# Kernel tuning notes

Measured on AMD Instinct MI355X. Metric: run time of the kernel, lower is better.

The kernel has to match this reference:

```python
import jax, jax.numpy as jnp
import numpy as np
from jax import lax

N = 100000   # n_nodes
E = 600000   # n_edges (no self loops by construction)
D = 128      # hidden_dim
L = 3        # n_hops
K = 5        # tail_k_threshold


def setup_inputs() -> dict:
    key = jax.random.key(0)
    ks = jax.random.split(key, 10)
    x = jax.random.normal(ks[0], (N, D), dtype=jnp.float32)
    src = jax.random.randint(ks[1], (E,), 0, N)
    off = jax.random.randint(ks[2], (E,), 1, N)
    dst = (src + off) % N  # guarantees dst != src (self loops removed in original)
    s = 1.0 / np.sqrt(D)
    def U(k, shape):
        return jax.random.uniform(k, shape, minval=-s, maxval=s, dtype=jnp.float32)
    return {
        "x": x,
        "G1": U(ks[3], (L, D, D)), "G2": U(ks[4], (L, D, D)),
        "B1": U(ks[5], (L, D, D)), "B2": U(ks[6], (L, D, D)),
        "R": U(ks[7], (L, D)),
        "edge_src": src, "edge_dst": dst,
    }


def _lrelu(v):
    return jax.nn.leaky_relu(v, 0.2)


def reference(x, G1, G2, B1, B2, R, edge_src, edge_dst):
    # row degrees of adj (A[src, dst] = 1)
    deg = jax.ops.segment_sum(jnp.ones(E, jnp.float32), edge_src, num_segments=N)
    inv_d = jnp.where(deg > 0, 1.0 / jnp.maximum(deg, 1.0), 0.0)   # left norm D^-1 A
    inv_d1 = 1.0 / (deg + 1.0)                                      # (A+I) left norm
    inv_d2 = 1.0 / (deg + 2.0)                                      # +1 virtual node
    w0, w1, w2 = inv_d[edge_src], inv_d1[edge_src], inv_d2[edge_src]
    head_mask = deg > K

    def spmm(w_edge, h):  # (D^-1 A) @ h via gather-scale-scatter
        return jax.ops.segment_sum(w_edge[:, None] * h[edge_dst], edge_src, num_segments=N)

    def propagate(head):
        h = x
        embs = [h]
        sups = []
        for l in range(L):
            nb = spmm(w0, h)
            ft = lax.stop_gradient(h)
            nbd = lax.stop_gradient(nb)
            gamma = _lrelu(ft @ G1[l].T + nbd @ G2[l].T) + 1.0
            beta = _lrelu(ft @ B1[l].T + nbd @ B2[l].T)
            m = ft + gamma * R[l] + beta - nbd   # missing_info (Relation, ablation=0)
            sups.append(m)
            if head:
                h = spmm(w1, h) + inv_d1[:, None] * h
            else:
                h = spmm(w2, h) + inv_d2[:, None] * h + m * inv_d2[:, None]
            embs.append(h)
        emb = jnp.mean(jnp.stack(embs, 0), 0)
        sup = jnp.mean(jnp.stack(sups, 0), 0)
        return emb, sup

    emb_h, _ = propagate(True)
    emb_t, _ = propagate(False)
    node_emb = jnp.where(head_mask[:, None], emb_h, emb_t)
    return node_emb
```

## Files before the change

kernel.cpp:

```cpp
#include <hip/hip_runtime.h>

#define N_NODES 100000
#define N_EDGES 600000
#define DIM 128
#define SCAN_B 1024
#define NCHUNK 98

typedef __attribute__((ext_vector_type(4))) float f32x4;
typedef __attribute__((ext_vector_type(8))) short bf16x8;
typedef __attribute__((ext_vector_type(4))) unsigned short u16x4;
typedef __attribute__((ext_vector_type(8))) unsigned short u16x8;

__device__ __forceinline__ unsigned short f2bf(float f) {
    union { float f; unsigned u; } cv; cv.f = f;
    unsigned r = (cv.u + 0x7FFFu + ((cv.u >> 16) & 1u)) >> 16;
    return (unsigned short)r;
}
__device__ __forceinline__ float bf2f(unsigned short v) {
    union { unsigned u; float f; } c; c.u = ((unsigned)v) << 16; return c.f;
}


__global__ void k_degree(const int* __restrict__ src, int* __restrict__ degi) {
    int e = blockIdx.x * 256 + threadIdx.x;
    if (e < N_EDGES) atomicAdd(&degi[src[e]], 1);
}

__global__ void k_chunksum(const int* __restrict__ degi, int* __restrict__ bsum) {
    __shared__ int sm[SCAN_B];
    int i = blockIdx.x * SCAN_B + threadIdx.x;
    sm[threadIdx.x] = (i < N_NODES) ? degi[i] : 0;
    __syncthreads();
    for (int s = SCAN_B / 2; s > 0; s >>= 1) {
        if (threadIdx.x < (unsigned)s) sm[threadIdx.x] += sm[threadIdx.x + s];
        __syncthreads();
    }
    if (threadIdx.x == 0) bsum[blockIdx.x] = sm[0];
}

__global__ void k_scanb(int* __restrict__ bsum, int nb) {
    __shared__ int sm[128];
    int t = threadIdx.x;
    int v = (t < nb) ? bsum[t] : 0;
    sm[t] = v; __syncthreads();
    for (int s = 1; s < 128; s <<= 1) {
        int a = (t >= s) ? sm[t - s] : 0;
        __syncthreads();
        sm[t] += a;
        __syncthreads();
    }
    if (t < nb) bsum[t] = sm[t] - v;
}

__global__ void k_rowptr(const int* __restrict__ degi, const int* __restrict__ bsum,
                         int* __restrict__ rowptr, int* __restrict__ cnt,
                         float* __restrict__ inv0, float* __restrict__ inv1,
                         float* __restrict__ inv2) {
    __shared__ int sm[SCAN_B];
    int i = blockIdx.x * SCAN_B + threadIdx.x;
    int v = (i < N_NODES) ? degi[i] : 0;
    sm[threadIdx.x] = v; __syncthreads();
    for (int s = 1; s < SCAN_B; s <<= 1) {
        int a = (threadIdx.x >= (unsigned)s) ? sm[threadIdx.x - s] : 0;
        __syncthreads();
        sm[threadIdx.x] += a;
        __syncthreads();
    }
    if (i < N_NODES) {
        int excl = bsum[blockIdx.x] + sm[threadIdx.x] - v;
        rowptr[i] = excl;
        cnt[i] = excl;
        float d = (float)v;
        inv0[i] = (v > 0) ? 1.0f / d : 0.0f;
        inv1[i] = 1.0f / (d + 1.0f);
        inv2[i] = 1.0f / (d + 2.0f);
    }
}

__global__ void k_fill(const int* __restrict__ src, const int* __restrict__ dst,
                       int* __restrict__ cnt, int* __restrict__ col) {
    int e = blockIdx.x * 256 + threadIdx.x;
    if (e < N_EDGES) {
        int pos = atomicAdd(&cnt[src[e]], 1);
        col[pos] = dst[e];
    }
}

__global__ void k_pack(const float* __restrict__ G1, const float* __restrict__ G2,
                       const float* __restrict__ B1, const float* __restrict__ B2,
                       short* __restrict__ Wp) {
    int idx = blockIdx.x * 256 + threadIdx.x;
    int j = idx & 7, lane = (idx >> 3) & 63, nt = (idx >> 9) & 15, kb = (idx >> 13) & 7, l = idx >> 16;
    int k = kb * 32 + (lane >> 4) * 8 + j;
    int n = nt * 16 + (lane & 15);
    float v;
    if (n < 128) {
        v = (k < 128) ? G1[(l * 128 + n) * 128 + k] : G2[(l * 128 + n) * 128 + (k - 128)];
    } else {
        int n2 = n - 128;
        v = (k < 128) ? B1[(l * 128 + n2) * 128 + k] : B2[(l * 128 + n2) * 128 + (k - 128)];
    }
    Wp[idx] = (short)f2bf(v);
}

__global__ void k_xcast(const float* __restrict__ x, unsigned short* __restrict__ xb) {
    int i = (blockIdx.x * 256 + threadIdx.x) * 4;
    f32x4 v = *(const f32x4*)(x + i);
    unsigned short o0 = f2bf(v[0]), o1 = f2bf(v[1]), o2 = f2bf(v[2]), o3 = f2bf(v[3]);
    unsigned long long pk = (unsigned long long)o0 | ((unsigned long long)o1 << 16)
                          | ((unsigned long long)o2 << 32) | ((unsigned long long)o3 << 48);
    *(unsigned long long*)(xb + i) = pk;
}


template <int NE>
__device__ __forceinline__ void gath_issue(const u16x8* __restrict__ h8,
        int idx, int base, int c, int d, float* acc) {
    u16x8 v[NE];
#pragma unroll
    for (int e = 0; e < NE; ++e) {
        int ce = __shfl(idx, base + e, 64);
        v[e] = h8[(size_t)ce * 16 + c];
    }
#pragma unroll
    for (int e = 0; e < NE; ++e) {
        if (e < d) {
#pragma unroll
            for (int j = 0; j < 8; ++j) acc[j] += bf2f(v[e][j]);
        }
    }
}

__device__ __forceinline__ void gather4(const u16x8* __restrict__ h8,
        const int* __restrict__ col, int start, int d, int lane, float* acc) {
    int c = lane & 15;
    int base = lane & 48;
    int dd = d < 16 ? d : 16;
    int idx = (c < dd) ? col[start + c] : 0;
    int dm = d;
    int tmx = __shfl_xor(dm, 16);
    dm = dm > tmx ? dm : tmx;
    tmx = __shfl_xor(dm, 32);
    dm = dm > tmx ? dm : tmx;
    if (dm <= 8) {
        gath_issue<8>(h8, idx, base, c, d, acc);
    } else {
        gath_issue<16>(h8, idx, base, c, d, acc);
        if (dm > 16) {
            for (int e = 16; e < d; ++e) {
                int c0 = col[start + e];
                u16x8 v = h8[(size_t)c0 * 16 + c];
#pragma unroll
                for (int j = 0; j < 8; ++j) acc[j] += bf2f(v[j]);
            }
        }
    }
}


__device__ __forceinline__ void tail_block(
    int rb,
    unsigned short (*sH)[136], unsigned short (*sS)[136], unsigned short (*sO)[136],
    const unsigned short* __restrict__ hb,
    unsigned short* __restrict__ hA, int write_hA,
    unsigned short* __restrict__ hb_next,
    const unsigned short* __restrict__ xb, const unsigned short* __restrict__ t1b,
    float* __restrict__ outp,
    const float* __restrict__ Rl, const short* __restrict__ Wp,
    const float* __restrict__ inv0, const float* __restrict__ inv1,
    const float* __restrict__ inv2,
    const int* __restrict__ rowptr, const int* __restrict__ degi,
    const int* __restrict__ col, int last)
{
    int wave = threadIdx.x >> 6, lane = threadIdx.x & 63;

    {
        int g = lane >> 4, c = lane & 15;
        int row = rb + wave * 4 + g;
        int start = rowptr[row], d = degi[row];
        u16x8 hv = ((const u16x8*)hb)[(size_t)row * 16 + c];
        float acc[8] = {0,0,0,0,0,0,0,0};
        gather4((const u16x8*)hb, col, start, d, lane, acc);
        u16x8 so;
#pragma unroll
        for (int j = 0; j < 8; ++j) so[j] = f2bf(acc[j]);
        *(u16x8*)&sS[wave * 4 + g][c * 8] = so;
        *(u16x8*)&sH[wave * 4 + g][c * 8] = hv;
        if (write_hA) {
            float w1 = inv1[row];
            u16x8 ho;
#pragma unroll
            for (int j = 0; j < 8; ++j) ho[j] = f2bf(w1 * (acc[j] + bf2f(hv[j])));
            ((u16x8*)hA)[(size_t)row * 16 + c] = ho;
        }
    }
    __syncthreads();

    int q = lane >> 4, m = lane & 15;
    float w0 = inv0[rb + m];
    const short* wl = Wp + lane * 8;

    const f32x4 vz = {0.f, 0.f, 0.f, 0.f};
    f32x4 aA[2] = {vz, vz}, aB[2] = {vz, vz};

#pragma unroll
    for (int kb = 0; kb < 4; ++kb) {
        bf16x8 ah = *(const bf16x8*)&sH[m][kb * 32 + q * 8];
#pragma unroll
        for (int j = 0; j < 2; ++j) {
            bf16x8 b1v = *(const bf16x8*)(wl + (kb * 16 + 2 * wave + j) * 512);
            bf16x8 b2v = *(const bf16x8*)(wl + (kb * 16 + 2 * wave + 8 + j) * 512);
            aA[j] = __builtin_amdgcn_mfma_f32_16x16x32_bf16(ah, b1v, aA[j], 0, 0, 0);
            aB[j] = __builtin_amdgcn_mfma_f32_16x16x32_bf16(ah, b2v, aB[j], 0, 0, 0);
        }
    }
#pragma unroll
    for (int kb = 0; kb < 4; ++kb) {
        u16x8 sv = *(const u16x8*)&sS[m][kb * 32 + q * 8];
        bf16x8 as;
#pragma unroll
        for (int j = 0; j < 8; ++j) as[j] = (short)f2bf(w0 * bf2f(sv[j]));
#pragma unroll
        for (int j = 0; j < 2; ++j) {
            bf16x8 b1v = *(const bf16x8*)(wl + ((kb + 4) * 16 + 2 * wave + j) * 512);
            bf16x8 b2v = *(const bf16x8*)(wl + ((kb + 4) * 16 + 2 * wave + 8 + j) * 512);
            aA[j] = __builtin_amdgcn_mfma_f32_16x16x32_bf16(as, b1v, aA[j], 0, 0, 0);
            aB[j] = __builtin_amdgcn_mfma_f32_16x16x32_bf16(as, b2v, aB[j], 0, 0, 0);
        }
    }

    float Rv[2];
#pragma unroll
    for (int j = 0; j < 2; ++j) Rv[j] = Rl[(2 * wave + j) * 16 + m];

#pragma unroll
    for (int r = 0; r < 4; ++r) {
        int gi = rb + q * 4 + r;
        float wi0 = inv0[gi], wi2 = inv2[gi];
        int dgi = degi[gi];
#pragma unroll
        for (int j = 0; j < 2; ++j) {
            int cc = (2 * wave + j) * 16 + m;
            float z1 = aA[j][r], z2 = aB[j][r];
            float h = bf2f(sH[q * 4 + r][cc]);
            float sva = bf2f(sS[q * 4 + r][cc]);
            float ga = (z1 > 0.f ? z1 : 0.2f * z1) + 1.0f;
            float be = (z2 > 0.f ? z2 : 0.2f * z2);
            float mm = h + ga * Rv[j] + be - wi0 * sva;
            float hn = wi2 * (sva + h + mm);
            if (!last) {
                sO[q * 4 + r][cc] = f2bf(hn);
            } else if (dgi <= 5) {
                float xv = bf2f(xb[(size_t)gi * DIM + cc]);
                float t1 = bf2f(t1b[(size_t)gi * DIM + cc]);
                outp[(size_t)gi * DIM + cc] = 0.25f * (xv + t1 + h + hn);
            }
        }
    }
    if (!last) {
        __syncthreads();
        int g = lane >> 4, c = lane & 15;
        int row = rb + wave * 4 + g;
        ((u16x8*)hb_next)[(size_t)row * 16 + c] = *(u16x8*)&sO[wave * 4 + g][c * 8];
    }
}

__device__ __forceinline__ void head_block(
    int rb,
    const unsigned short* __restrict__ hsrc, unsigned short* __restrict__ hnext,
    const unsigned short* __restrict__ xb, const unsigned short* __restrict__ h1b,
    float* __restrict__ outp, const float* __restrict__ inv1,
    const int* __restrict__ rowptr, const int* __restrict__ degi,
    const int* __restrict__ col, int final_hop)
{
    int wave = threadIdx.x >> 6, lane = threadIdx.x & 63;
    int g = lane >> 4, c = lane & 15;
    int row = rb + wave * 4 + g;
    int start = rowptr[row], d = degi[row];
    u16x8 hv = ((const u16x8*)hsrc)[(size_t)row * 16 + c];
    float acc[8] = {0,0,0,0,0,0,0,0};
    gather4((const u16x8*)hsrc, col, start, d, lane, acc);
    float w = inv1[row];
    float hn[8];
#pragma unroll
    for (int j = 0; j < 8; ++j) hn[j] = w * (acc[j] + bf2f(hv[j]));
    if (!final_hop) {
        u16x8 ho;
#pragma unroll
        for (int j = 0; j < 8; ++j) ho[j] = f2bf(hn[j]);
        ((u16x8*)hnext)[(size_t)row * 16 + c] = ho;
    } else if (d > 5) {
        u16x8 xv = ((const u16x8*)xb)[(size_t)row * 16 + c];
        u16x8 h1 = ((const u16x8*)h1b)[(size_t)row * 16 + c];
        f32x4 e0, e1;
#pragma unroll
        for (int j = 0; j < 4; ++j)
            e0[j] = 0.25f * (bf2f(xv[j]) + bf2f(h1[j]) + bf2f(hv[j]) + hn[j]);
#pragma unroll
        for (int j = 0; j < 4; ++j)
            e1[j] = 0.25f * (bf2f(xv[4 + j]) + bf2f(h1[4 + j]) + bf2f(hv[4 + j]) + hn[4 + j]);
        float* op = outp + (size_t)row * DIM + c * 8;
        *(f32x4*)op = e0;
        *(f32x4*)(op + 4) = e1;
    }
}


__global__ __launch_bounds__(256, 4) void k_fused0(
    const unsigned short* __restrict__ xb, unsigned short* __restrict__ hA,
    unsigned short* __restrict__ tA, float* __restrict__ outp,
    const float* __restrict__ Rl, const short* __restrict__ Wp,
    const float* __restrict__ inv0, const float* __restrict__ inv1,
    const float* __restrict__ inv2,
    const int* __restrict__ rowptr, const int* __restrict__ degi,
    const int* __restrict__ col)
{
    __shared__ __align__(16) unsigned short sH[16][136], sS[16][136], sO[16][136];
    tail_block(blockIdx.x * 16, sH, sS, sO, xb, hA, 1, tA, xb, tA, outp,
               Rl, Wp, inv0, inv1, inv2, rowptr, degi, col, 0);
}

__global__ __launch_bounds__(256, 4) void k_tail(
    const unsigned short* __restrict__ tb, unsigned short* __restrict__ tb_next,
    const unsigned short* __restrict__ xb, const unsigned short* __restrict__ t1b,
    float* __restrict__ outp,
    const float* __restrict__ Rl, const short* __restrict__ Wp,
    const float* __restrict__ inv0, const float* __restrict__ inv1,
    const float* __restrict__ inv2,
    const int* __restrict__ rowptr, const int* __restrict__ degi,
    const int* __restrict__ col, int last)
{
    __shared__ __align__(16) unsigned short sH[16][136], sS[16][136], sO[16][136];
    tail_block(blockIdx.x * 16, sH, sS, sO, tb, (unsigned short*)0, 0, tb_next,
               xb, t1b, outp, Rl, Wp, inv0, inv1, inv2, rowptr, degi, col, last);
}

__global__ __launch_bounds__(256, 4) void k_head(
    const unsigned short* __restrict__ hsrc, unsigned short* __restrict__ hnext,
    const unsigned short* __restrict__ xb, const unsigned short* __restrict__ h1b,
    float* __restrict__ outp, const float* __restrict__ inv1,
    const int* __restrict__ rowptr, const int* __restrict__ degi,
    const int* __restrict__ col, int final_hop)
{
    head_block(blockIdx.x * 16, hsrc, hnext, xb, h1b, outp, inv1,
               rowptr, degi, col, final_hop);
}


extern "C" void kernel_launch(void* const* d_in, const int* in_sizes, int n_in,
                              void* d_out, int out_size, void* d_ws, size_t ws_size,
                              hipStream_t stream) {
    const float* x  = (const float*)d_in[0];
    const float* G1 = (const float*)d_in[1];
    const float* G2 = (const float*)d_in[2];
    const float* B1 = (const float*)d_in[3];
    const float* B2 = (const float*)d_in[4];
    const float* R  = (const float*)d_in[5];
    const int* esrc = (const int*)d_in[6];
    const int* edst = (const int*)d_in[7];
    float* out = (float*)d_out;

    char* base = (char*)d_ws;
    size_t off = 0;
    auto alloc = [&](size_t b) -> void* {
        void* p = base + off;
        off = (off + b + 255) & ~(size_t)255;
        return p;
    };
    int* degi   = (int*)alloc(4 * N_NODES);
    int* rowptr = (int*)alloc(4 * N_NODES);
    int* cnt    = (int*)alloc(4 * N_NODES);
    int* bsum   = (int*)alloc(4 * 256);
    int* col    = (int*)alloc(4 * N_EDGES);
    float* inv0 = (float*)alloc(4 * N_NODES);
    float* inv1 = (float*)alloc(4 * N_NODES);
    float* inv2 = (float*)alloc(4 * N_NODES);
    short* Wp   = (short*)alloc(2 * 3 * 65536);
    unsigned short* xb = (unsigned short*)alloc(2ull * N_NODES * DIM);
    unsigned short* hA = (unsigned short*)alloc(2ull * N_NODES * DIM);
    unsigned short* hB = (unsigned short*)alloc(2ull * N_NODES * DIM);
    unsigned short* tA = (unsigned short*)alloc(2ull * N_NODES * DIM);
    unsigned short* tB = (unsigned short*)alloc(2ull * N_NODES * DIM);

    hipMemsetAsync(degi, 0, 4 * N_NODES, stream);
    k_degree<<<(N_EDGES + 255) / 256, 256, 0, stream>>>(esrc, degi);
    k_chunksum<<<NCHUNK, SCAN_B, 0, stream>>>(degi, bsum);
    k_scanb<<<1, 128, 0, stream>>>(bsum, NCHUNK);
    k_rowptr<<<NCHUNK, SCAN_B, 0, stream>>>(degi, bsum, rowptr, cnt, inv0, inv1, inv2);
    k_fill<<<(N_EDGES + 255) / 256, 256, 0, stream>>>(esrc, edst, cnt, col);
    k_pack<<<768, 256, 0, stream>>>(G1, G2, B1, B2, Wp);
    k_xcast<<<12500, 256, 0, stream>>>(x, xb);

    k_fused0<<<6250, 256, 0, stream>>>(xb, hA, tA, out, R, Wp,
                                       inv0, inv1, inv2, rowptr, degi, col);

    k_head<<<6250, 256, 0, stream>>>(hA, hB, xb, hA, out, inv1, rowptr, degi, col, 0);
    k_head<<<6250, 256, 0, stream>>>(hB, hB, xb, hA, out, inv1, rowptr, degi, col, 1);

    k_tail<<<6250, 256, 0, stream>>>(tA, tB, xb, tA, out, R + 128, Wp + 65536,
                                     inv0, inv1, inv2, rowptr, degi, col, 0);
    k_tail<<<6250, 256, 0, stream>>>(tB, tB, xb, tA, out, R + 256, Wp + 131072,
                                     inv0, inv1, inv2, rowptr, degi, col, 1);
}
```

Before: 403.7 us.

## Fuse head and tail hop kernels into one dual-gather kernel per hop

Merges the separate head and tail propagation kernels for hops 2 and 3 into a single kernel that gathers neighbour rows from both the head and tail buffers using the same column indices. This shares the CSR index loads and rowptr/degree reads and cuts kernel launches from four to two. The cost is doubled register pressure in the gather (two accumulator sets and two loaded vectors per edge), which may lower occupancy. In-place reuse of tB/hB on the last hop is avoided by passing null next-buffers.

```diff
diff --git a/kernel.cpp b/kernel.cpp
--- a/kernel.cpp
+++ b/kernel.cpp
@@ -157,45 +157,73 @@
     }
 }
 
-
-__device__ __forceinline__ void tail_block(
+template <int NE>
+__device__ __forceinline__ void gath_issue2(const u16x8* __restrict__ hT,
+        const u16x8* __restrict__ hH,
+        int idx, int base, int c, int d, int e0, float* accT, float* accH) {
+    u16x8 vT[NE], vH[NE];
+#pragma unroll
+    for (int e = 0; e < NE; ++e) {
+        int ce = __shfl(idx, base + e0 + e, 64);
+        vT[e] = hT[(size_t)ce * 16 + c];
+        vH[e] = hH[(size_t)ce * 16 + c];
+    }
+#pragma unroll
+    for (int e = 0; e < NE; ++e) {
+        if (e0 + e < d) {
+#pragma unroll
+            for (int j = 0; j < 8; ++j) {
+                accT[j] += bf2f(vT[e][j]);
+                accH[j] += bf2f(vH[e][j]);
+            }
+        }
+    }
+}
+
+__device__ __forceinline__ void gather4_dual(const u16x8* __restrict__ hT,
+        const u16x8* __restrict__ hH,
+        const int* __restrict__ col, int start, int d, int lane,
+        float* accT, float* accH) {
+    int c = lane & 15;
+    int base = lane & 48;
+    int dd = d < 16 ? d : 16;
+    int idx = (c < dd) ? col[start + c] : 0;
+    int dm = d;
+    int tmx = __shfl_xor(dm, 16);
+    dm = dm > tmx ? dm : tmx;
+    tmx = __shfl_xor(dm, 32);
+    dm = dm > tmx ? dm : tmx;
+    if (dm <= 8) {
+        gath_issue2<8>(hT, hH, idx, base, c, d, 0, accT, accH);
+    } else {
+        gath_issue2<8>(hT, hH, idx, base, c, d, 0, accT, accH);
+        gath_issue2<8>(hT, hH, idx, base, c, d, 8, accT, accH);
+        if (dm > 16) {
+            for (int e = 16; e < d; ++e) {
+                int c0 = col[start + e];
+                u16x8 vT = hT[(size_t)c0 * 16 + c];
+                u16x8 vH = hH[(size_t)c0 * 16 + c];
+#pragma unroll
+                for (int j = 0; j < 8; ++j) {
+                    accT[j] += bf2f(vT[j]);
+                    accH[j] += bf2f(vH[j]);
+                }
+            }
+        }
+    }
+}
+
+__device__ __forceinline__ void tail_gemm(
     int rb,
     unsigned short (*sH)[136], unsigned short (*sS)[136], unsigned short (*sO)[136],
-    const unsigned short* __restrict__ hb,
-    unsigned short* __restrict__ hA, int write_hA,
     unsigned short* __restrict__ hb_next,
     const unsigned short* __restrict__ xb, const unsigned short* __restrict__ t1b,
     float* __restrict__ outp,
     const float* __restrict__ Rl, const short* __restrict__ Wp,
-    const float* __restrict__ inv0, const float* __restrict__ inv1,
-    const float* __restrict__ inv2,
-    const int* __restrict__ rowptr, const int* __restrict__ degi,
-    const int* __restrict__ col, int last)
+    const float* __restrict__ inv0, const float* __restrict__ inv2,
+    const int* __restrict__ degi, int last)
 {
     int wave = threadIdx.x >> 6, lane = threadIdx.x & 63;
-
-    {
-        int g = lane >> 4, c = lane & 15;
-        int row = rb + wave * 4 + g;
-        int start = rowptr[row], d = degi[row];
-        u16x8 hv = ((const u16x8*)hb)[(size_t)row * 16 + c];
-        float acc[8] = {0,0,0,0,0,0,0,0};
-        gather4((const u16x8*)hb, col, start, d, lane, acc);
-        u16x8 so;
-#pragma unroll
-        for (int j = 0; j < 8; ++j) so[j] = f2bf(acc[j]);
-        *(u16x8*)&sS[wave * 4 + g][c * 8] = so;
-        *(u16x8*)&sH[wave * 4 + g][c * 8] = hv;
-        if (write_hA) {
-            float w1 = inv1[row];
-            u16x8 ho;
-#pragma unroll
-            for (int j = 0; j < 8; ++j) ho[j] = f2bf(w1 * (acc[j] + bf2f(hv[j])));
-            ((u16x8*)hA)[(size_t)row * 16 + c] = ho;
-        }
-    }
-    __syncthreads();
-
     int q = lane >> 4, m = lane & 15;
     float w0 = inv0[rb + m];
     const short* wl = Wp + lane * 8;
@@ -265,46 +293,6 @@
     }
 }
 
-__device__ __forceinline__ void head_block(
-    int rb,
-    const unsigned short* __restrict__ hsrc, unsigned short* __restrict__ hnext,
-    const unsigned short* __restrict__ xb, const unsigned short* __restrict__ h1b,
-    float* __restrict__ outp, const float* __restrict__ inv1,
-    const int* __restrict__ rowptr, const int* __restrict__ degi,
-    const int* __restrict__ col, int final_hop)
-{
-    int wave = threadIdx.x >> 6, lane = threadIdx.x & 63;
-    int g = lane >> 4, c = lane & 15;
-    int row = rb + wave * 4 + g;
-    int start = rowptr[row], d = degi[row];
-    u16x8 hv = ((const u16x8*)hsrc)[(size_t)row * 16 + c];
-    float acc[8] = {0,0,0,0,0,0,0,0};
-    gather4((const u16x8*)hsrc, col, start, d, lane, acc);
-    float w = inv1[row];
-    float hn[8];
-#pragma unroll
-    for (int j = 0; j < 8; ++j) hn[j] = w * (acc[j] + bf2f(hv[j]));
-    if (!final_hop) {
-        u16x8 ho;
-#pragma unroll
-        for (int j = 0; j < 8; ++j) ho[j] = f2bf(hn[j]);
-        ((u16x8*)hnext)[(size_t)row * 16 + c] = ho;
-    } else if (d > 5) {
-        u16x8 xv = ((const u16x8*)xb)[(size_t)row * 16 + c];
-        u16x8 h1 = ((const u16x8*)h1b)[(size_t)row * 16 + c];
-        f32x4 e0, e1;
-#pragma unroll
-        for (int j = 0; j < 4; ++j)
-            e0[j] = 0.25f * (bf2f(xv[j]) + bf2f(h1[j]) + bf2f(hv[j]) + hn[j]);
-#pragma unroll
-        for (int j = 0; j < 4; ++j)
-            e1[j] = 0.25f * (bf2f(xv[4 + j]) + bf2f(h1[4 + j]) + bf2f(hv[4 + j]) + hn[4 + j]);
-        float* op = outp + (size_t)row * DIM + c * 8;
-        *(f32x4*)op = e0;
-        *(f32x4*)(op + 4) = e1;
-    }
-}
-
 
 __global__ __launch_bounds__(256, 4) void k_fused0(
     const unsigned short* __restrict__ xb, unsigned short* __restrict__ hA,
@@ -316,14 +304,35 @@
     const int* __restrict__ col)
 {
     __shared__ __align__(16) unsigned short sH[16][136], sS[16][136], sO[16][136];
-    tail_block(blockIdx.x * 16, sH, sS, sO, xb, hA, 1, tA, xb, tA, outp,
-               Rl, Wp, inv0, inv1, inv2, rowptr, degi, col, 0);
-}
-
-__global__ __launch_bounds__(256, 4) void k_tail(
+    int rb = blockIdx.x * 16;
+    int wave = threadIdx.x >> 6, lane = threadIdx.x & 63;
+    {
+        int g = lane >> 4, c = lane & 15;
+        int row = rb + wave * 4 + g;
+        int start = rowptr[row], d = degi[row];
+        u16x8 hv = ((const u16x8*)xb)[(size_t)row * 16 + c];
+        float acc[8] = {0,0,0,0,0,0,0,0};
+        gather4((const u16x8*)xb, col, start, d, lane, acc);
+        u16x8 so;
+#pragma unroll
+        for (int j = 0; j < 8; ++j) so[j] = f2bf(acc[j]);
+        *(u16x8*)&sS[wave * 4 + g][c * 8] = so;
+        *(u16x8*)&sH[wave * 4 + g][c * 8] = hv;
+        float w1 = inv1[row];
+        u16x8 ho;
+#pragma unroll
+        for (int j = 0; j < 8; ++j) ho[j] = f2bf(w1 * (acc[j] + bf2f(hv[j])));
+        ((u16x8*)hA)[(size_t)row * 16 + c] = ho;
+    }
+    __syncthreads();
+    tail_gemm(rb, sH, sS, sO, tA, xb, tA, outp, Rl, Wp, inv0, inv2, degi, 0);
+}
+
+__global__ __launch_bounds__(256, 4) void k_hop(
     const unsigned short* __restrict__ tb, unsigned short* __restrict__ tb_next,
+    const unsigned short* __restrict__ hb, unsigned short* __restrict__ hb_next,
     const unsigned short* __restrict__ xb, const unsigned short* __restrict__ t1b,
-    float* __restrict__ outp,
+    const unsigned short* __restrict__ h1b, float* __restrict__ outp,
     const float* __restrict__ Rl, const short* __restrict__ Wp,
     const float* __restrict__ inv0, const float* __restrict__ inv1,
     const float* __restrict__ inv2,
@@ -331,19 +340,53 @@
     const int* __restrict__ col, int last)
 {
     __shared__ __align__(16) unsigned short sH[16][136], sS[16][136], sO[16][136];
-    tail_block(blockIdx.x * 16, sH, sS, sO, tb, (unsigned short*)0, 0, tb_next,
-               xb, t1b, outp, Rl, Wp, inv0, inv1, inv2, rowptr, degi, col, last);
-}
-
-__global__ __launch_bounds__(256, 4) void k_head(
-    const unsigned short* __restrict__ hsrc, unsigned short* __restrict__ hnext,
-    const unsigned short* __restrict__ xb, const unsigned short* __restrict__ h1b,
-    float* __restrict__ outp, const float* __restrict__ inv1,
-    const int* __restrict__ rowptr, const int* __restrict__ degi,
-    const int* __restrict__ col, int final_hop)
-{
-    head_block(blockIdx.x * 16, hsrc, hnext, xb, h1b, outp, inv1,
-               rowptr, degi, col, final_hop);
+    int rb = blockIdx.x * 16;
+    int wave = threadIdx.x >> 6, lane = threadIdx.x & 63;
+
+    {
+        int g = lane >> 4, c = lane & 15;
+        int row = rb + wave * 4 + g;
+        int start = rowptr[row], d = degi[row];
+        u16x8 tv = ((const u16x8*)tb)[(size_t)row * 16 + c];
+        u16x8 hv = ((const u16x8*)hb)[(size_t)row * 16 + c];
+        float accT[8] = {0,0,0,0,0,0,0,0};
+        float accH[8] = {0,0,0,0,0,0,0,0};
+        gather4_dual((const u16x8*)tb, (const u16x8*)hb, col, start, d, lane, accT, accH);
+
+        u16x8 so;
+#pragma unroll
+        for (int j = 0; j < 8; ++j) so[j] = f2bf(accT[j]);
+        *(u16x8*)&sS[wave * 4 + g][c * 8] = so;
+        *(u16x8*)&sH[wave * 4 + g][c * 8] = tv;
+
+        float w1 = inv1[row];
+        if (!last) {
+            u16x8 ho;
+#pragma unroll
+            for (int j = 0; j < 8; ++j) ho[j] = f2bf(w1 * (accH[j] + bf2f(hv[j])));
+            ((u16x8*)hb_next)[(size_t)row * 16 + c] = ho;
+        } else if (d > 5) {
+            u16x8 xv = ((const u16x8*)xb)[(size_t)row * 16 + c];
+            u16x8 h1 = ((const u16x8*)h1b)[(size_t)row * 16 + c];
+            f32x4 e0, e1;
+#pragma unroll
+            for (int j = 0; j < 4; ++j) {
+                float h2 = bf2f(hv[j]);
+                e0[j] = 0.25f * (bf2f(xv[j]) + bf2f(h1[j]) + h2 + w1 * (accH[j] + h2));
+            }
+#pragma unroll
+            for (int j = 0; j < 4; ++j) {
+                float h2 = bf2f(hv[4 + j]);
+                e1[j] = 0.25f * (bf2f(xv[4 + j]) + bf2f(h1[4 + j]) + h2 + w1 * (accH[4 + j] + h2));
+            }
+            float* op = outp + (size_t)row * DIM + c * 8;
+            *(f32x4*)op = e0;
+            *(f32x4*)(op + 4) = e1;
+        }
+    }
+    __syncthreads();
+
+    tail_gemm(rb, sH, sS, sO, tb_next, xb, t1b, outp, Rl, Wp, inv0, inv2, degi, last);
 }
 
 
@@ -394,11 +437,12 @@
     k_fused0<<<6250, 256, 0, stream>>>(xb, hA, tA, out, R, Wp,
                                        inv0, inv1, inv2, rowptr, degi, col);
 
-    k_head<<<6250, 256, 0, stream>>>(hA, hB, xb, hA, out, inv1, rowptr, degi, col, 0);
-    k_head<<<6250, 256, 0, stream>>>(hB, hB, xb, hA, out, inv1, rowptr, degi, col, 1);
-
-    k_tail<<<6250, 256, 0, stream>>>(tA, tB, xb, tA, out, R + 128, Wp + 65536,
-                                     inv0, inv1, inv2, rowptr, degi, col, 0);
-    k_tail<<<6250, 256, 0, stream>>>(tB, tB, xb, tA, out, R + 256, Wp + 131072,
-                                     inv0, inv1, inv2, rowptr, degi, col, 1);
-}
+    k_hop<<<6250, 256, 0, stream>>>(tA, tB, hA, hB, xb, tA, hA, out,
+                                    R + 128, Wp + 65536,
+                                    inv0, inv1, inv2, rowptr, degi, col, 0);
+
+    k_hop<<<6250, 256, 0, stream>>>(tB, (unsigned short*)0, hB, (unsigned short*)0,
+                                    xb, tA, hA, out,
+                                    R + 256, Wp + 131072,
+                                    inv0, inv1, inv2, rowptr, degi, col, 1);
+}
```

Result: no change. 397.2 us (-1.6%).
